# Performance work log

Measured on AMD Instinct MI355X. Metric: run time of the kernel, lower is better.

The kernel has to match this reference:

```python
import jax, jax.numpy as jnp
import numpy as np

D_MODEL = 1024
NUM_HEADS = 16
D_K = D_MODEL // NUM_HEADS
THETA = 10000.0


def _rope(x, pos):
    # x: [H, B, S, D_K]; pos: [S] int. Interleaved-pair rotation (matrix-form RoPE).
    d2 = D_K // 2
    inv_freq = THETA ** (-(2.0 * jnp.arange(d2, dtype=jnp.float32)) / D_K)  # [d2]
    ang = pos.astype(jnp.float32)[:, None] * inv_freq[None, :]              # [S, d2]
    sin, cos = jnp.sin(ang), jnp.cos(ang)
    xr = x.reshape(*x.shape[:-1], d2, 2)
    x0, x1 = xr[..., 0], xr[..., 1]
    out0 = cos * x0 - sin * x1
    out1 = sin * x0 + cos * x1
    return jnp.stack([out0, out1], axis=-1).reshape(x.shape)


def setup_inputs() -> dict:
    key = jax.random.key(0)
    ks = jax.random.split(key, 5)
    scale = 1.0 / np.sqrt(D_MODEL)
    return {
        "x": jax.random.normal(ks[0], (4, 2048, D_MODEL), dtype=jnp.float32),
        "token_positions": jnp.arange(2048, dtype=jnp.int32),
        "Wq": jax.random.normal(ks[1], (D_MODEL, D_MODEL), dtype=jnp.float32) * scale,
        "Wk": jax.random.normal(ks[2], (D_MODEL, D_MODEL), dtype=jnp.float32) * scale,
        "Wv": jax.random.normal(ks[3], (D_MODEL, D_MODEL), dtype=jnp.float32) * scale,
        "Wo": jax.random.normal(ks[4], (D_MODEL, D_MODEL), dtype=jnp.float32) * scale,
    }


def reference(x, token_positions, Wq, Wk, Wv, Wo):
    B, S, D = x.shape
    H, dk = NUM_HEADS, D_K
    # Projections (Linear stores weight [out,in], applies x @ W.T)
    def proj(W):
        return (x @ W.T).reshape(B, S, H, dk).transpose(2, 0, 1, 3)  # [H,B,S,dk]
    q, k, v = proj(Wq), proj(Wk), proj(Wv)
    q = _rope(q, token_positions)
    k = _rope(k, token_positions)
    scores = jnp.einsum("hbsd,hbtd->hbst", q, k) / jnp.sqrt(jnp.float32(dk))
    causal = jnp.tril(jnp.ones((S, S), dtype=bool))
    scores = jnp.where(causal, scores, jnp.float32(-1e9))
    attn = jax.nn.softmax(scores, axis=-1)
    out = jnp.einsum("hbst,hbtd->hbsd", attn, v)       # [H,B,S,dk]
    out = out.transpose(1, 2, 0, 3).reshape(B, S, D)   # [B,S,D]
    return out @ Wo.T
```

## Files before the change

kernel.cpp:

```cpp
#include <hip/hip_runtime.h>

typedef __bf16 bf16;
typedef bf16 bf16x8 __attribute__((ext_vector_type(8)));
typedef bf16 bf16x4 __attribute__((ext_vector_type(4)));
typedef float floatx4 __attribute__((ext_vector_type(4)));

#define D_MODEL 1024
#define SEQ     2048
#define NB      4
#define NH      16
#define DKH     64
#define ROPE_L2 0.4152410118609203f

__device__ __forceinline__ floatx4 mfma16(bf16x8 a, bf16x8 b, floatx4 c) {
  return __builtin_amdgcn_mfma_f32_16x16x32_bf16(a, b, c, 0, 0, 0);
}

__device__ __forceinline__ void gload_lds16(void* lds_uniform, const void* gsrc) {
  __builtin_amdgcn_global_load_lds(
      (__attribute__((address_space(1))) unsigned int*)(void*)(gsrc),
      (__attribute__((address_space(3))) unsigned int*)lds_uniform,
      16, 0, 0);
}

__global__ __launch_bounds__(256) void cvt_all(
    const float4* __restrict__ x,
    const float4* __restrict__ wq, const float4* __restrict__ wk,
    const float4* __restrict__ wv, const float4* __restrict__ wo,
    bf16x4* __restrict__ xb,
    bf16x4* __restrict__ b0, bf16x4* __restrict__ b1,
    bf16x4* __restrict__ b2, bf16x4* __restrict__ b3,
    const int* __restrict__ tokpos, float2* __restrict__ ropetab) {
  const int i = blockIdx.x * 256 + threadIdx.x;
  if (i < (1 << 21) + (1 << 20)) {
    const float4* src;
    bf16x4* dst;
    int off;
    if (i < (1 << 21)) {
      src = x; dst = xb; off = i;
    } else {
      const int j = i - (1 << 21);
      const int widx = j >> 18;
      off = j & ((1 << 18) - 1);
      src = (widx == 0) ? wq : (widx == 1) ? wk : (widx == 2) ? wv : wo;
      dst = (widx == 0) ? b0 : (widx == 1) ? b1 : (widx == 2) ? b2 : b3;
    }
    const float4 v = src[off];
    bf16x4 o;
    o[0] = (bf16)v.x; o[1] = (bf16)v.y; o[2] = (bf16)v.z; o[3] = (bf16)v.w;
    dst[off] = o;
  } else {
    const int k = i - (1 << 21) - (1 << 20);
    const int s = k >> 5, i2 = k & 31;
    const float ang = (float)tokpos[s] * exp2f(-(float)i2 * ROPE_L2);
    float sn, cs;
    sincosf(ang, &sn, &cs);
    ropetab[k] = make_float2(sn, cs);
  }
}

#define QK_SRC_DECL(Aptr, Bq, Bk)                                              \
  const int c_0 = w * 64 + lane;                                               \
  const int row0_ = c_0 >> 2, seg0_ = (c_0 & 3) ^ ((row0_ >> 1) & 3);          \
  const int c_1 = c_0 + 256;                                                   \
  const int row1_ = c_1 >> 2, seg1_ = (c_1 & 3) ^ ((row1_ >> 1) & 3);          \
  const bf16* asrc0 = (Aptr) + (size_t)(bm + row0_) * D_MODEL + seg0_ * 8;     \
  const bf16* asrc1 = (Aptr) + (size_t)(bm + row1_) * D_MODEL + seg1_ * 8;     \
  const bf16* bqsrc0 = (Bq) + (size_t)(bn + row0_) * D_MODEL + seg0_ * 8;      \
  const bf16* bqsrc1 = (Bq) + (size_t)(bn + row1_) * D_MODEL + seg1_ * 8;      \
  const bf16* bksrc0 = (Bk) + (size_t)(bn + row0_) * D_MODEL + seg0_ * 8;      \
  const bf16* bksrc1 = (Bk) + (size_t)(bn + row1_) * D_MODEL + seg1_ * 8;     \
  const int gsw = (g ^ ((r >> 1) & 3)) * 8;

#define QKA(buf) ((char*)LDSBUF + (buf) * 8192)
#define QKQ(buf) ((char*)LDSBUF + 16384 + (buf) * 8192)
#define QKK(buf) ((char*)LDSBUF + 32768 + (buf) * 8192)

#define QK_STAGE(buf, kk)                                                      \
  gload_lds16(QKA(buf) + (w * 64) * 16, asrc0 + (kk));                         \
  gload_lds16(QKQ(buf) + (w * 64) * 16, bqsrc0 + (kk));                        \
  gload_lds16(QKK(buf) + (w * 64) * 16, bksrc0 + (kk));                        \
  gload_lds16(QKA(buf) + (w * 64 + 256) * 16, asrc1 + (kk));                   \
  gload_lds16(QKQ(buf) + (w * 64 + 256) * 16, bqsrc1 + (kk));                  \
  gload_lds16(QKK(buf) + (w * 64 + 256) * 16, bksrc1 + (kk));

#define ROPEW(mm, nn, CV, SC)                                                  \
  _Pragma("unroll")                                                            \
  for (int reg = 0; reg < 4; ++reg) {                                          \
    const int srow = mm * 16 + g * 4 + reg;                                    \
    const int c = wc * 64 + nn * 16 + r;                                       \
    const int s_ = (bm + wr * 64 + srow) & (SEQ - 1);                          \
    const int d_ = c & 63;                                                     \
    float v = CV[reg];                                                         \
    float pp = __shfl_xor(v, 1);                                               \
    const float2 sc2 = ropetab[s_ * 32 + (d_ >> 1)];                           \
    float res = ((d_ & 1) == 0) ? (sc2.y * v - sc2.x * pp)                     \
                                : (sc2.x * pp + sc2.y * v);                    \
    res *= SC;                                                                 \
    *(bf16*)((char*)LDSBUF + srow * 272 + c * 2) = (bf16)res;                  \
  }

#define QK_EPI(A00,A01,A02,A03,A10,A11,A12,A13,A20,A21,A22,A23,A30,A31,A32,A33,\
               dst0, SC)                                                       \
  _Pragma("unroll")                                                            \
  for (int p = 0; p < 2; ++p) {                                                \
    if (wr == p) {                                                             \
      ROPEW(0, 0, A00, SC) ROPEW(0, 1, A01, SC) ROPEW(0, 2, A02, SC)           \
      ROPEW(0, 3, A03, SC) ROPEW(1, 0, A10, SC) ROPEW(1, 1, A11, SC)           \
      ROPEW(1, 2, A12, SC) ROPEW(1, 3, A13, SC) ROPEW(2, 0, A20, SC)           \
      ROPEW(2, 1, A21, SC) ROPEW(2, 2, A22, SC) ROPEW(2, 3, A23, SC)           \
      ROPEW(3, 0, A30, SC) ROPEW(3, 1, A31, SC) ROPEW(3, 2, A32, SC)           \
      ROPEW(3, 3, A33, SC)                                                     \
    }                                                                          \
    __syncthreads();                                                           \
    const int s_r = tid >> 2, quad = tid & 3;                                  \
    const int grow = bm + p * 64 + s_r;                                        \
    const int b_ = grow >> 11, s_ = grow & (SEQ - 1);                          \
    const int h_ = hbase + (quad >> 1);                                        \
    bf16* dstp = (dst0) + ((size_t)(b_ * NH + h_) * SEQ + s_) * DKH +          \
                 (quad & 1) * 32;                                              \
    _Pragma("unroll")                                                          \
    for (int j = 0; j < 4; ++j)                                                \
      *(float4*)(dstp + j * 8) =                                               \
          *(const float4*)((char*)LDSBUF + s_r * 272 + quad * 64 + j * 16);    \
    __syncthreads();                                                           \
  }

#define AS_BASE(buf) ((char*)LDSBUF + (buf) * 8192)
#define BS_BASE(buf) ((char*)LDSBUF + 16384 + (buf) * 8192)

#define GEMM_STAGE(buf, kk)                                                    \
  gload_lds16(AS_BASE(buf) + (w * 64) * 16, asrc0 + (kk));                     \
  gload_lds16(BS_BASE(buf) + (w * 64) * 16, bsrc0 + (kk));                     \
  gload_lds16(AS_BASE(buf) + (w * 64 + 256) * 16, asrc1 + (kk));               \
  gload_lds16(BS_BASE(buf) + (w * 64 + 256) * 16, bsrc1 + (kk));

#define GEMM_MAINLOOP(Aptr, Bptr)                                              \
  const int c_0 = w * 64 + lane;                                               \
  const int row0_ = c_0 >> 2, seg0_ = (c_0 & 3) ^ ((row0_ >> 1) & 3);          \
  const int c_1 = c_0 + 256;                                                   \
  const int row1_ = c_1 >> 2, seg1_ = (c_1 & 3) ^ ((row1_ >> 1) & 3);          \
  const bf16* asrc0 = (Aptr) + (size_t)(bm + row0_) * D_MODEL + seg0_ * 8;     \
  const bf16* asrc1 = (Aptr) + (size_t)(bm + row1_) * D_MODEL + seg1_ * 8;     \
  const bf16* bsrc0 = (Bptr) + (size_t)(bn + row0_) * D_MODEL + seg0_ * 8;     \
  const bf16* bsrc1 = (Bptr) + (size_t)(bn + row1_) * D_MODEL + seg1_ * 8;     \
  const int gsw = (g ^ ((r >> 1) & 3)) * 8;                                    \
  GEMM_STAGE(0, 0)                                                             \
  __syncthreads();                                                             \
  int cub = 0;                                                                 \
  for (int kt = 0; kt < 32; ++kt) {                                            \
    if (kt + 1 < 32) { GEMM_STAGE(cub ^ 1, (kt + 1) * 32) }                    \
    const bf16* Abase = (const bf16*)AS_BASE(cub) + (wr * 64 + r) * 32 + gsw;  \
    const bf16* Bbase = (const bf16*)BS_BASE(cub) + (wc * 64 + r) * 32 + gsw;  \
    bf16x8 a0 = *(const bf16x8*)(Abase + 0 * 512);                             \
    bf16x8 a1 = *(const bf16x8*)(Abase + 1 * 512);                             \
    bf16x8 a2 = *(const bf16x8*)(Abase + 2 * 512);                             \
    bf16x8 a3 = *(const bf16x8*)(Abase + 3 * 512);                             \
    bf16x8 b0 = *(const bf16x8*)(Bbase + 0 * 512);                             \
    bf16x8 b1 = *(const bf16x8*)(Bbase + 1 * 512);                             \
    bf16x8 b2 = *(const bf16x8*)(Bbase + 2 * 512);                             \
    bf16x8 b3 = *(const bf16x8*)(Bbase + 3 * 512);                             \
    __builtin_amdgcn_s_setprio(1);                                             \
    c00 = mfma16(a0, b0, c00); c01 = mfma16(a0, b1, c01);                      \
    c02 = mfma16(a0, b2, c02); c03 = mfma16(a0, b3, c03);                      \
    c10 = mfma16(a1, b0, c10); c11 = mfma16(a1, b1, c11);                      \
    c12 = mfma16(a1, b2, c12); c13 = mfma16(a1, b3, c13);                      \
    c20 = mfma16(a2, b0, c20); c21 = mfma16(a2, b1, c21);                      \
    c22 = mfma16(a2, b2, c22); c23 = mfma16(a2, b3, c23);                      \
    c30 = mfma16(a3, b0, c30); c31 = mfma16(a3, b1, c31);                      \
    c32 = mfma16(a3, b2, c32); c33 = mfma16(a3, b3, c33);                      \
    __builtin_amdgcn_s_setprio(0);                                             \
    __syncthreads();                                                           \
    cub ^= 1;                                                                  \
  }

#define V_WRITE(mm, nn, CV)                                                    \
  _Pragma("unroll")                                                            \
  for (int reg = 0; reg < 4; ++reg) {                                          \
    const int crow = nn * 16 + r;                                              \
    const int s_l = wr * 64 + mm * 16 + g * 4 + reg;                           \
    *(bf16*)((char*)LDSBUF + crow * 272 + s_l * 2) = (bf16)CV[reg];            \
  }

__global__ __launch_bounds__(256, 2) void gemm_proj(
    const bf16* __restrict__ A,
    const bf16* __restrict__ Wq, const bf16* __restrict__ Wk,
    const bf16* __restrict__ Wv,
    bf16* __restrict__ Qd, bf16* __restrict__ Kd, bf16* __restrict__ Vd,
    const float2* __restrict__ ropetab) {
  __shared__ __align__(16) char LDSBUF[49152];
  const int orig = (int)(blockIdx.x + (blockIdx.y << 3));
  const int l = (orig & 7) * 64 + (orig >> 3);
  const int bm = (l >> 3) * 128, bn = (l & 7) * 128;
  const int tid = threadIdx.x, lane = tid & 63, w = tid >> 6;
  const int wr = w >> 1, wc = w & 1;
  const int r = lane & 15, g = lane >> 4;
  const int hbase = bn >> 6;

  if (blockIdx.z == 0) {
    floatx4 q00 = {}, q01 = {}, q02 = {}, q03 = {};
    floatx4 q10 = {}, q11 = {}, q12 = {}, q13 = {};
    floatx4 q20 = {}, q21 = {}, q22 = {}, q23 = {};
    floatx4 q30 = {}, q31 = {}, q32 = {}, q33 = {};
    floatx4 k00 = {}, k01 = {}, k02 = {}, k03 = {};
    floatx4 k10 = {}, k11 = {}, k12 = {}, k13 = {};
    floatx4 k20 = {}, k21 = {}, k22 = {}, k23 = {};
    floatx4 k30 = {}, k31 = {}, k32 = {}, k33 = {};

    QK_SRC_DECL(A, Wq, Wk)
    QK_STAGE(0, 0)
    __syncthreads();
    int cub = 0;
    for (int kt = 0; kt < 32; ++kt) {
      if (kt + 1 < 32) { QK_STAGE(cub ^ 1, (kt + 1) * 32) }
      const bf16* Abase = (const bf16*)QKA(cub) + (wr * 64 + r) * 32 + gsw;
      const bf16* Qbase = (const bf16*)QKQ(cub) + (wc * 64 + r) * 32 + gsw;
      const bf16* Kbase = (const bf16*)QKK(cub) + (wc * 64 + r) * 32 + gsw;
      bf16x8 a0 = *(const bf16x8*)(Abase + 0 * 512);
      bf16x8 a1 = *(const bf16x8*)(Abase + 1 * 512);
      bf16x8 a2 = *(const bf16x8*)(Abase + 2 * 512);
      bf16x8 a3 = *(const bf16x8*)(Abase + 3 * 512);
      bf16x8 bq0 = *(const bf16x8*)(Qbase + 0 * 512);
      bf16x8 bq1 = *(const bf16x8*)(Qbase + 1 * 512);
      bf16x8 bq2 = *(const bf16x8*)(Qbase + 2 * 512);
      bf16x8 bq3 = *(const bf16x8*)(Qbase + 3 * 512);
      bf16x8 bk0 = *(const bf16x8*)(Kbase + 0 * 512);
      bf16x8 bk1 = *(const bf16x8*)(Kbase + 1 * 512);
      bf16x8 bk2 = *(const bf16x8*)(Kbase + 2 * 512);
      bf16x8 bk3 = *(const bf16x8*)(Kbase + 3 * 512);
      __builtin_amdgcn_s_setprio(1);
      q00 = mfma16(a0, bq0, q00); q01 = mfma16(a0, bq1, q01);
      q02 = mfma16(a0, bq2, q02); q03 = mfma16(a0, bq3, q03);
      k00 = mfma16(a0, bk0, k00); k01 = mfma16(a0, bk1, k01);
      k02 = mfma16(a0, bk2, k02); k03 = mfma16(a0, bk3, k03);
      q10 = mfma16(a1, bq0, q10); q11 = mfma16(a1, bq1, q11);
      q12 = mfma16(a1, bq2, q12); q13 = mfma16(a1, bq3, q13);
      k10 = mfma16(a1, bk0, k10); k11 = mfma16(a1, bk1, k11);
      k12 = mfma16(a1, bk2, k12); k13 = mfma16(a1, bk3, k13);
      q20 = mfma16(a2, bq0, q20); q21 = mfma16(a2, bq1, q21);
      q22 = mfma16(a2, bq2, q22); q23 = mfma16(a2, bq3, q23);
      k20 = mfma16(a2, bk0, k20); k21 = mfma16(a2, bk1, k21);
      k22 = mfma16(a2, bk2, k22); k23 = mfma16(a2, bk3, k23);
      q30 = mfma16(a3, bq0, q30); q31 = mfma16(a3, bq1, q31);
      q32 = mfma16(a3, bq2, q32); q33 = mfma16(a3, bq3, q33);
      k30 = mfma16(a3, bk0, k30); k31 = mfma16(a3, bk1, k31);
      k32 = mfma16(a3, bk2, k32); k33 = mfma16(a3, bk3, k33);
      __builtin_amdgcn_s_setprio(0);
      __syncthreads();
      cub ^= 1;
    }

    QK_EPI(q00,q01,q02,q03,q10,q11,q12,q13,q20,q21,q22,q23,q30,q31,q32,q33,
           Qd, 0.125f)
    QK_EPI(k00,k01,k02,k03,k10,k11,k12,k13,k20,k21,k22,k23,k30,k31,k32,k33,
           Kd, 1.0f)
  } else {
    floatx4 c00 = {}, c01 = {}, c02 = {}, c03 = {};
    floatx4 c10 = {}, c11 = {}, c12 = {}, c13 = {};
    floatx4 c20 = {}, c21 = {}, c22 = {}, c23 = {};
    floatx4 c30 = {}, c31 = {}, c32 = {}, c33 = {};
    GEMM_MAINLOOP(A, Wv)

    const int b_ = bm >> 11, sbase = bm & (SEQ - 1);
#pragma unroll
    for (int p = 0; p < 2; ++p) {
      if (wc == p) {
        V_WRITE(0, 0, c00) V_WRITE(0, 1, c01) V_WRITE(0, 2, c02) V_WRITE(0, 3, c03)
        V_WRITE(1, 0, c10) V_WRITE(1, 1, c11) V_WRITE(1, 2, c12) V_WRITE(1, 3, c13)
        V_WRITE(2, 0, c20) V_WRITE(2, 1, c21) V_WRITE(2, 2, c22) V_WRITE(2, 3, c23)
        V_WRITE(3, 0, c30) V_WRITE(3, 1, c31) V_WRITE(3, 2, c32) V_WRITE(3, 3, c33)
      }
      __syncthreads();
      const int c_r = tid >> 2, quad = tid & 3;
      const int c = p * 64 + c_r;
      const int h_ = hbase + (c >> 6), d_ = c & 63;
      bf16* dstp = Vd + ((size_t)(b_ * NH + h_) * DKH + d_) * SEQ + sbase + quad * 32;
#pragma unroll
      for (int j = 0; j < 4; ++j)
        *(float4*)(dstp + j * 8) =
            *(const float4*)((char*)LDSBUF + c_r * 272 + quad * 64 + j * 16);
      __syncthreads();
    }
  }
}

#define OUT_EPI(mm, nn, CV)                                                    \
  _Pragma("unroll")                                                            \
  for (int reg = 0; reg < 4; ++reg) {                                          \
    const int grow = bm + wr * 64 + mm * 16 + g * 4 + reg;                     \
    const int gcol = bn + wc * 64 + nn * 16 + r;                               \
    C[(size_t)grow * D_MODEL + gcol] = CV[reg];                                \
  }

__global__ __launch_bounds__(256, 3) void gemm_out(const bf16* __restrict__ A,
                                                   const bf16* __restrict__ Bw,
                                                   float* __restrict__ C) {
  __shared__ __align__(16) char LDSBUF[32768];
  const int orig = (int)(blockIdx.x + (blockIdx.y << 3));
  const int l = (orig & 7) * 64 + (orig >> 3);
  const int bm = (l >> 3) * 128, bn = (l & 7) * 128;
  const int tid = threadIdx.x, lane = tid & 63, w = tid >> 6;
  const int wr = w >> 1, wc = w & 1;
  const int r = lane & 15, g = lane >> 4;
  floatx4 c00 = {}, c01 = {}, c02 = {}, c03 = {};
  floatx4 c10 = {}, c11 = {}, c12 = {}, c13 = {};
  floatx4 c20 = {}, c21 = {}, c22 = {}, c23 = {};
  floatx4 c30 = {}, c31 = {}, c32 = {}, c33 = {};
  GEMM_MAINLOOP(A, Bw)
  OUT_EPI(0, 0, c00) OUT_EPI(0, 1, c01) OUT_EPI(0, 2, c02) OUT_EPI(0, 3, c03)
  OUT_EPI(1, 0, c10) OUT_EPI(1, 1, c11) OUT_EPI(1, 2, c12) OUT_EPI(1, 3, c13)
  OUT_EPI(2, 0, c20) OUT_EPI(2, 1, c21) OUT_EPI(2, 2, c22) OUT_EPI(2, 3, c23)
  OUT_EPI(3, 0, c30) OUT_EPI(3, 1, c31) OUT_EPI(3, 2, c32) OUT_EPI(3, 3, c33)
}

__global__ __launch_bounds__(256, 3) void attn128(const bf16* __restrict__ Q,
                                                  const bf16* __restrict__ Kk,
                                                  const bf16* __restrict__ Vt,
                                                  bf16* __restrict__ AO) {
  const int orig = (int)(blockIdx.x + (blockIdx.y << 4));
  const int i_ = orig >> 3;
  const int qt = 15 - (i_ >> 3);
  const int bh = (orig & 7) * 8 + (i_ & 7);
  const int b = bh >> 4, h = bh & 15;
  const int tid = threadIdx.x, lane = tid & 63, w = tid >> 6;
  const int r = lane & 15, g = lane >> 4;
  const int q0 = qt * 128 + w * 32;

  const bf16* Qb = Q + (size_t)bh * SEQ * DKH;
  const bf16* Kb = Kk + (size_t)bh * SEQ * DKH;
  const bf16* Vb = Vt + (size_t)bh * DKH * SEQ;

  __shared__ bf16 Ks[2][64 * 64];
  __shared__ bf16 Vs[2][64 * 64];
  __shared__ bf16 Ps[4][32 * 64];

  int ldsoff[2];
  const char* ksrc[2];
  const char* vsrc[2];
#pragma unroll
  for (int j = 0; j < 2; ++j) {
    const int L = (w * 64 + lane + 256 * j) * 16;
    const int S = L ^ (((L >> 7) & 7) << 4);
    ldsoff[j] = (w * 64 + 256 * j) * 16;
    ksrc[j] = (const char*)Kb + S;
    vsrc[j] = (const char*)Vb + (size_t)(S >> 7) * (SEQ * 2) + (S & 127);
  }

#define ATTN_STAGE(buf, tt)                                                   \
  _Pragma("unroll")                                                           \
  for (int j = 0; j < 2; ++j) {                                               \
    gload_lds16((char*)Ks[buf] + ldsoff[j], ksrc[j] + (size_t)(tt) * 8192);   \
    gload_lds16((char*)Vs[buf] + ldsoff[j], vsrc[j] + (size_t)(tt) * 128);    \
  }

#define SM_TILE(MASKED)                                                        \
  _Pragma("unroll")                                                            \
  for (int m = 0; m < 2; ++m) {                                                \
    const int qq_ = q0 + m * 16 + r;                                           \
    const int wl_ = m * 16 + r;                                                \
    _Pragma("unroll")                                                          \
    for (int nf = 0; nf < 4; ++nf) {                                           \
      floatx4 p;                                                               \
      _Pragma("unroll")                                                        \
      for (int reg = 0; reg < 4; ++reg) {                                      \
        float pe = exp2f(fmaf(sc[m][nf][reg], 1.442695041f, -17.31234049f));   \
        if (MASKED && (t0 + nf * 16 + g * 4 + reg > qq_)) pe = 0.f;            \
        p[reg] = pe;                                                           \
      }                                                                        \
      l2[m] += p;                                                              \
      unsigned u0, u1;                                                         \
      asm("v_cvt_pk_bf16_f32 %0, %1, %2" : "=v"(u0) : "v"(p[0]), "v"(p[1]));   \
      asm("v_cvt_pk_bf16_f32 %0, %1, %2" : "=v"(u1) : "v"(p[2]), "v"(p[3]));   \
      const int pb = (wl_ * 128 + nf * 32 + g * 8) ^ ((wl_ & 7) << 4);         \
      *(uint2*)((char*)Ps[w] + pb) = make_uint2(u0, u1);                       \
    }                                                                          \
  }

  bf16x8 qf[2][2];
#pragma unroll
  for (int m = 0; m < 2; ++m)
#pragma unroll
    for (int ks = 0; ks < 2; ++ks)
      qf[m][ks] = *(const bf16x8*)(Qb + (size_t)(q0 + m * 16 + r) * DKH + ks * 32 + g * 8);

  floatx4 o[2][4] = {};
  floatx4 l2[2] = {};

  const int nt = 2 * qt + 2;
  ATTN_STAGE(0, 0)
  __syncthreads();
  int cu = 0;
  for (int t = 0; t < nt; ++t) {
    if (t + 1 < nt) ATTN_STAGE(cu ^ 1, t + 1)
    const int t0 = t * 64;

    floatx4 sc[2][4];
    __builtin_amdgcn_s_setprio(1);
#pragma unroll
    for (int nf = 0; nf < 4; ++nf) {
      const int row = nf * 16 + r;
      const int off0 = (row * 128 + g * 16) ^ ((row & 7) << 4);
      bf16x8 kf0 = *(const bf16x8*)((const char*)Ks[cu] + off0);
      bf16x8 kf1 = *(const bf16x8*)((const char*)Ks[cu] + (off0 ^ 64));
      sc[0][nf] = mfma16(kf1, qf[0][1], mfma16(kf0, qf[0][0], floatx4{0.f, 0.f, 0.f, 0.f}));
      sc[1][nf] = mfma16(kf1, qf[1][1], mfma16(kf0, qf[1][0], floatx4{0.f, 0.f, 0.f, 0.f}));
    }
    __builtin_amdgcn_s_setprio(0);

    const bool edge = (t0 + 63 > q0);
    if (edge) {
      SM_TILE(1)
    } else {
      SM_TILE(0)
    }
    asm volatile("s_waitcnt lgkmcnt(0)" ::: "memory");

    bf16x8 pf[2][2];
#pragma unroll
    for (int m = 0; m < 2; ++m)
#pragma unroll
      for (int ks = 0; ks < 2; ++ks) {
        const int prow = m * 16 + r;
        const int ab = (prow * 128 + ks * 64 + g * 16) ^ ((prow & 7) << 4);
        pf[m][ks] = *(const bf16x8*)((const char*)Ps[w] + ab);
      }
    __builtin_amdgcn_s_setprio(1);
#pragma unroll
    for (int nf = 0; nf < 4; ++nf) {
      const int vrow = nf * 16 + r;
      const int vb0 = (vrow * 128 + g * 16) ^ ((vrow & 7) << 4);
      bf16x8 vf0 = *(const bf16x8*)((const char*)Vs[cu] + vb0);
      bf16x8 vf1 = *(const bf16x8*)((const char*)Vs[cu] + (vb0 ^ 64));
#pragma unroll
      for (int m = 0; m < 2; ++m)
        o[m][nf] = mfma16(pf[m][1], vf1, mfma16(pf[m][0], vf0, o[m][nf]));
    }
    __builtin_amdgcn_s_setprio(0);
    __syncthreads();
    cu ^= 1;
  }

  float lsm[2];
#pragma unroll
  for (int m = 0; m < 2; ++m) {
    float ls = l2[m][0] + l2[m][1] + l2[m][2] + l2[m][3];
    ls += __shfl_xor(ls, 16);
    ls += __shfl_xor(ls, 32);
    lsm[m] = ls;
  }
  float linv[2][4];
#pragma unroll
  for (int m = 0; m < 2; ++m)
#pragma unroll
    for (int reg = 0; reg < 4; ++reg)
      linv[m][reg] = 1.f / __shfl(lsm[m], g * 4 + reg);

#pragma unroll
  for (int m = 0; m < 2; ++m)
#pragma unroll
    for (int nf = 0; nf < 4; ++nf)
#pragma unroll
      for (int reg = 0; reg < 4; ++reg) {
        const int s = q0 + m * 16 + g * 4 + reg;
        const int d = nf * 16 + r;
        const float val = o[m][nf][reg] * linv[m][reg];
        AO[((size_t)(b * SEQ + s)) * D_MODEL + h * DKH + d] = (bf16)val;
      }
}

extern "C" void kernel_launch(void* const* d_in, const int* in_sizes, int n_in,
                              void* d_out, int out_size, void* d_ws, size_t ws_size,
                              hipStream_t stream) {
  const float* x = (const float*)d_in[0];
  const int* tokpos = (const int*)d_in[1];
  const float* Wq = (const float*)d_in[2];
  const float* Wk = (const float*)d_in[3];
  const float* Wv = (const float*)d_in[4];
  const float* Wo = (const float*)d_in[5];
  float* out = (float*)d_out;

  char* ws = (char*)d_ws;
  if (ws_size < (72ull << 20)) return;

  bf16* xb  = (bf16*)(ws);
  bf16* wb0 = (bf16*)(ws + (16ull << 20));
  bf16* wb1 = (bf16*)(ws + (18ull << 20));
  bf16* wb2 = (bf16*)(ws + (20ull << 20));
  bf16* wb3 = (bf16*)(ws + (22ull << 20));
  bf16* Qb  = (bf16*)(ws + (24ull << 20));
  bf16* Kb  = (bf16*)(ws + (40ull << 20));
  bf16* Vt  = (bf16*)(ws + (56ull << 20));
  bf16* AO  = (bf16*)(ws);
  float2* ropetab = (float2*)d_out;

  cvt_all<<<12544, 256, 0, stream>>>((const float4*)x, (const float4*)Wq,
                                     (const float4*)Wk, (const float4*)Wv,
                                     (const float4*)Wo, (bf16x4*)xb,
                                     (bf16x4*)wb0, (bf16x4*)wb1,
                                     (bf16x4*)wb2, (bf16x4*)wb3,
                                     tokpos, ropetab);

  gemm_proj<<<dim3(8, 64, 2), 256, 0, stream>>>(xb, wb0, wb1, wb2,
                                                Qb, Kb, Vt, ropetab);
  attn128<<<dim3(16, 64), 256, 0, stream>>>(Qb, Kb, Vt, AO);
  gemm_out<<<dim3(8, 64), 256, 0, stream>>>(AO, wb3, out);
}
```

Baseline: 171.3 us.

## Split fused QK projection into per-head 64-wide tiles to balance work with V blocks

The Q/K projection blocks now cover a 128x64 tile (one head) for both Wq and Wk instead of 128x128, so each QK block does the same MFMA work as a V block. The grid changes to a flat 1536-block launch in which two of every three blocks are QK blocks, with swizzled block indexing. LDS use drops from 48KB to 32KB, which can raise occupancy. The cost is that each A tile is loaded from memory twice as often for QK, and there are more blocks and epilogue barriers.

New measurement: 187.8 us. 9.6% more time.

```diff
diff --git a/kernel.cpp b/kernel.cpp
--- a/kernel.cpp
+++ b/kernel.cpp
@@ -59,70 +59,51 @@
   }
 }
 
-#define QK_SRC_DECL(Aptr, Bq, Bk)                                              \
-  const int c_0 = w * 64 + lane;                                               \
-  const int row0_ = c_0 >> 2, seg0_ = (c_0 & 3) ^ ((row0_ >> 1) & 3);          \
-  const int c_1 = c_0 + 256;                                                   \
-  const int row1_ = c_1 >> 2, seg1_ = (c_1 & 3) ^ ((row1_ >> 1) & 3);          \
-  const bf16* asrc0 = (Aptr) + (size_t)(bm + row0_) * D_MODEL + seg0_ * 8;     \
-  const bf16* asrc1 = (Aptr) + (size_t)(bm + row1_) * D_MODEL + seg1_ * 8;     \
-  const bf16* bqsrc0 = (Bq) + (size_t)(bn + row0_) * D_MODEL + seg0_ * 8;      \
-  const bf16* bqsrc1 = (Bq) + (size_t)(bn + row1_) * D_MODEL + seg1_ * 8;      \
-  const bf16* bksrc0 = (Bk) + (size_t)(bn + row0_) * D_MODEL + seg0_ * 8;      \
-  const bf16* bksrc1 = (Bk) + (size_t)(bn + row1_) * D_MODEL + seg1_ * 8;     \
-  const int gsw = (g ^ ((r >> 1) & 3)) * 8;
-
-#define QKA(buf) ((char*)LDSBUF + (buf) * 8192)
-#define QKQ(buf) ((char*)LDSBUF + 16384 + (buf) * 8192)
-#define QKK(buf) ((char*)LDSBUF + 32768 + (buf) * 8192)
-
-#define QK_STAGE(buf, kk)                                                      \
-  gload_lds16(QKA(buf) + (w * 64) * 16, asrc0 + (kk));                         \
-  gload_lds16(QKQ(buf) + (w * 64) * 16, bqsrc0 + (kk));                        \
-  gload_lds16(QKK(buf) + (w * 64) * 16, bksrc0 + (kk));                        \
-  gload_lds16(QKA(buf) + (w * 64 + 256) * 16, asrc1 + (kk));                   \
-  gload_lds16(QKQ(buf) + (w * 64 + 256) * 16, bqsrc1 + (kk));                  \
-  gload_lds16(QKK(buf) + (w * 64 + 256) * 16, bksrc1 + (kk));
-
-#define ROPEW(mm, nn, CV, SC)                                                  \
+
+#define QK64A(buf) ((char*)LDSBUF + (buf) * 16384)
+#define QK64Q(buf) ((char*)LDSBUF + (buf) * 16384 + 8192)
+#define QK64K(buf) ((char*)LDSBUF + (buf) * 16384 + 12288)
+
+#define QK64_STAGE(buf, kk)                                                    \
+  gload_lds16(QK64A(buf) + (w * 64) * 16, asrc0 + (kk));                       \
+  gload_lds16(QK64A(buf) + (w * 64 + 256) * 16, asrc1 + (kk));                 \
+  gload_lds16(QK64Q(buf) + (w * 64) * 16, bqsrc + (kk));                       \
+  gload_lds16(QK64K(buf) + (w * 64) * 16, bksrc + (kk));
+
+#define ROPEW64(mm, nn, CV, SC)                                                \
   _Pragma("unroll")                                                            \
   for (int reg = 0; reg < 4; ++reg) {                                          \
     const int srow = mm * 16 + g * 4 + reg;                                    \
-    const int c = wc * 64 + nn * 16 + r;                                       \
-    const int s_ = (bm + wr * 64 + srow) & (SEQ - 1);                          \
-    const int d_ = c & 63;                                                     \
+    const int col = wc * 32 + nn * 16 + r;                                     \
+    const int s_ = (bm + p * 64 + srow) & (SEQ - 1);                           \
     float v = CV[reg];                                                         \
     float pp = __shfl_xor(v, 1);                                               \
-    const float2 sc2 = ropetab[s_ * 32 + (d_ >> 1)];                           \
-    float res = ((d_ & 1) == 0) ? (sc2.y * v - sc2.x * pp)                     \
-                                : (sc2.x * pp + sc2.y * v);                    \
+    const float2 sc2 = ropetab[s_ * 32 + (col >> 1)];                          \
+    float res = ((col & 1) == 0) ? (sc2.y * v - sc2.x * pp)                    \
+                                 : (sc2.x * pp + sc2.y * v);                   \
     res *= SC;                                                                 \
-    *(bf16*)((char*)LDSBUF + srow * 272 + c * 2) = (bf16)res;                  \
-  }
-
-#define QK_EPI(A00,A01,A02,A03,A10,A11,A12,A13,A20,A21,A22,A23,A30,A31,A32,A33,\
-               dst0, SC)                                                       \
+    *(bf16*)((char*)LDSBUF + srow * 272 + col * 2) = (bf16)res;                \
+  }
+
+#define QK64_EPI(A00,A01,A10,A11,A20,A21,A30,A31, dst0, SC)                    \
   _Pragma("unroll")                                                            \
   for (int p = 0; p < 2; ++p) {                                                \
     if (wr == p) {                                                             \
-      ROPEW(0, 0, A00, SC) ROPEW(0, 1, A01, SC) ROPEW(0, 2, A02, SC)           \
-      ROPEW(0, 3, A03, SC) ROPEW(1, 0, A10, SC) ROPEW(1, 1, A11, SC)           \
-      ROPEW(1, 2, A12, SC) ROPEW(1, 3, A13, SC) ROPEW(2, 0, A20, SC)           \
-      ROPEW(2, 1, A21, SC) ROPEW(2, 2, A22, SC) ROPEW(2, 3, A23, SC)           \
-      ROPEW(3, 0, A30, SC) ROPEW(3, 1, A31, SC) ROPEW(3, 2, A32, SC)           \
-      ROPEW(3, 3, A33, SC)                                                     \
+      ROPEW64(0, 0, A00, SC) ROPEW64(0, 1, A01, SC)                            \
+      ROPEW64(1, 0, A10, SC) ROPEW64(1, 1, A11, SC)                            \
+      ROPEW64(2, 0, A20, SC) ROPEW64(2, 1, A21, SC)                            \
+      ROPEW64(3, 0, A30, SC) ROPEW64(3, 1, A31, SC)                            \
     }                                                                          \
     __syncthreads();                                                           \
     const int s_r = tid >> 2, quad = tid & 3;                                  \
     const int grow = bm + p * 64 + s_r;                                        \
     const int b_ = grow >> 11, s_ = grow & (SEQ - 1);                          \
-    const int h_ = hbase + (quad >> 1);                                        \
-    bf16* dstp = (dst0) + ((size_t)(b_ * NH + h_) * SEQ + s_) * DKH +          \
-                 (quad & 1) * 32;                                              \
+    bf16* dstp = (dst0) + ((size_t)(b_ * NH + h) * SEQ + s_) * DKH +           \
+                 quad * 16;                                                    \
     _Pragma("unroll")                                                          \
-    for (int j = 0; j < 4; ++j)                                                \
+    for (int j = 0; j < 2; ++j)                                                \
       *(float4*)(dstp + j * 8) =                                               \
-          *(const float4*)((char*)LDSBUF + s_r * 272 + quad * 64 + j * 16);    \
+          *(const float4*)((char*)LDSBUF + s_r * 272 + quad * 32 + j * 16);    \
     __syncthreads();                                                           \
   }
 
@@ -188,73 +169,71 @@
     const bf16* __restrict__ Wv,
     bf16* __restrict__ Qd, bf16* __restrict__ Kd, bf16* __restrict__ Vd,
     const float2* __restrict__ ropetab) {
-  __shared__ __align__(16) char LDSBUF[49152];
-  const int orig = (int)(blockIdx.x + (blockIdx.y << 3));
-  const int l = (orig & 7) * 64 + (orig >> 3);
-  const int bm = (l >> 3) * 128, bn = (l & 7) * 128;
+  __shared__ __align__(16) char LDSBUF[32768];
+  const int orig = (int)(blockIdx.x + (blockIdx.y << 4));
+  const int l = (orig & 7) * 192 + (orig >> 3);
+  const int grp = l / 3, rem = l - grp * 3;
   const int tid = threadIdx.x, lane = tid & 63, w = tid >> 6;
   const int wr = w >> 1, wc = w & 1;
   const int r = lane & 15, g = lane >> 4;
-  const int hbase = bn >> 6;
-
-  if (blockIdx.z == 0) {
-    floatx4 q00 = {}, q01 = {}, q02 = {}, q03 = {};
-    floatx4 q10 = {}, q11 = {}, q12 = {}, q13 = {};
-    floatx4 q20 = {}, q21 = {}, q22 = {}, q23 = {};
-    floatx4 q30 = {}, q31 = {}, q32 = {}, q33 = {};
-    floatx4 k00 = {}, k01 = {}, k02 = {}, k03 = {};
-    floatx4 k10 = {}, k11 = {}, k12 = {}, k13 = {};
-    floatx4 k20 = {}, k21 = {}, k22 = {}, k23 = {};
-    floatx4 k30 = {}, k31 = {}, k32 = {}, k33 = {};
-
-    QK_SRC_DECL(A, Wq, Wk)
-    QK_STAGE(0, 0)
+
+  if (rem < 2) {
+    const int id = grp * 2 + rem;
+    const int bm = (id >> 4) * 128;
+    const int h = id & 15;
+    const int bn = h * 64;
+
+    const int ar0 = tid >> 2, as0 = (tid & 3) ^ ((ar0 >> 1) & 3);
+    const int cA1 = tid + 256;
+    const int ar1 = cA1 >> 2, as1 = (cA1 & 3) ^ ((ar1 >> 1) & 3);
+    const bf16* asrc0 = A + (size_t)(bm + ar0) * D_MODEL + as0 * 8;
+    const bf16* asrc1 = A + (size_t)(bm + ar1) * D_MODEL + as1 * 8;
+    const int br = tid >> 2, bs = (tid & 3) ^ ((br >> 1) & 3);
+    const bf16* bqsrc = Wq + (size_t)(bn + br) * D_MODEL + bs * 8;
+    const bf16* bksrc = Wk + (size_t)(bn + br) * D_MODEL + bs * 8;
+    const int gsw = (g ^ ((r >> 1) & 3)) * 8;
+
+    floatx4 q00 = {}, q01 = {}, q10 = {}, q11 = {};
+    floatx4 q20 = {}, q21 = {}, q30 = {}, q31 = {};
+    floatx4 k00 = {}, k01 = {}, k10 = {}, k11 = {};
+    floatx4 k20 = {}, k21 = {}, k30 = {}, k31 = {};
+
+    QK64_STAGE(0, 0)
     __syncthreads();
     int cub = 0;
     for (int kt = 0; kt < 32; ++kt) {
-      if (kt + 1 < 32) { QK_STAGE(cub ^ 1, (kt + 1) * 32) }
-      const bf16* Abase = (const bf16*)QKA(cub) + (wr * 64 + r) * 32 + gsw;
-      const bf16* Qbase = (const bf16*)QKQ(cub) + (wc * 64 + r) * 32 + gsw;
-      const bf16* Kbase = (const bf16*)QKK(cub) + (wc * 64 + r) * 32 + gsw;
+      if (kt + 1 < 32) { QK64_STAGE(cub ^ 1, (kt + 1) * 32) }
+      const bf16* Abase = (const bf16*)QK64A(cub) + (wr * 64 + r) * 32 + gsw;
+      const bf16* Qbase = (const bf16*)QK64Q(cub) + (wc * 32 + r) * 32 + gsw;
+      const bf16* Kbase = (const bf16*)QK64K(cub) + (wc * 32 + r) * 32 + gsw;
       bf16x8 a0 = *(const bf16x8*)(Abase + 0 * 512);
       bf16x8 a1 = *(const bf16x8*)(Abase + 1 * 512);
       bf16x8 a2 = *(const bf16x8*)(Abase + 2 * 512);
       bf16x8 a3 = *(const bf16x8*)(Abase + 3 * 512);
       bf16x8 bq0 = *(const bf16x8*)(Qbase + 0 * 512);
       bf16x8 bq1 = *(const bf16x8*)(Qbase + 1 * 512);
-      bf16x8 bq2 = *(const bf16x8*)(Qbase + 2 * 512);
-      bf16x8 bq3 = *(const bf16x8*)(Qbase + 3 * 512);
       bf16x8 bk0 = *(const bf16x8*)(Kbase + 0 * 512);
       bf16x8 bk1 = *(const bf16x8*)(Kbase + 1 * 512);
-      bf16x8 bk2 = *(const bf16x8*)(Kbase + 2 * 512);
-      bf16x8 bk3 = *(const bf16x8*)(Kbase + 3 * 512);
       __builtin_amdgcn_s_setprio(1);
       q00 = mfma16(a0, bq0, q00); q01 = mfma16(a0, bq1, q01);
-      q02 = mfma16(a0, bq2, q02); q03 = mfma16(a0, bq3, q03);
       k00 = mfma16(a0, bk0, k00); k01 = mfma16(a0, bk1, k01);
-      k02 = mfma16(a0, bk2, k02); k03 = mfma16(a0, bk3, k03);
       q10 = mfma16(a1, bq0, q10); q11 = mfma16(a1, bq1, q11);
-      q12 = mfma16(a1, bq2, q12); q13 = mfma16(a1, bq3, q13);
       k10 = mfma16(a1, bk0, k10); k11 = mfma16(a1, bk1, k11);
-      k12 = mfma16(a1, bk2, k12); k13 = mfma16(a1, bk3, k13);
       q20 = mfma16(a2, bq0, q20); q21 = mfma16(a2, bq1, q21);
-      q22 = mfma16(a2, bq2, q22); q23 = mfma16(a2, bq3, q23);
       k20 = mfma16(a2, bk0, k20); k21 = mfma16(a2, bk1, k21);
-      k22 = mfma16(a2, bk2, k22); k23 = mfma16(a2, bk3, k23);
       q30 = mfma16(a3, bq0, q30); q31 = mfma16(a3, bq1, q31);
-      q32 = mfma16(a3, bq2, q32); q33 = mfma16(a3, bq3, q33);
       k30 = mfma16(a3, bk0, k30); k31 = mfma16(a3, bk1, k31);
-      k32 = mfma16(a3, bk2, k32); k33 = mfma16(a3, bk3, k33);
       __builtin_amdgcn_s_setprio(0);
       __syncthreads();
       cub ^= 1;
     }
 
-    QK_EPI(q00,q01,q02,q03,q10,q11,q12,q13,q20,q21,q22,q23,q30,q31,q32,q33,
-           Qd, 0.125f)
-    QK_EPI(k00,k01,k02,k03,k10,k11,k12,k13,k20,k21,k22,k23,k30,k31,k32,k33,
-           Kd, 1.0f)
+    QK64_EPI(q00, q01, q10, q11, q20, q21, q30, q31, Qd, 0.125f)
+    QK64_EPI(k00, k01, k10, k11, k20, k21, k30, k31, Kd, 1.0f)
   } else {
+    const int id = grp;
+    const int bm = (id >> 3) * 128, bn = (id & 7) * 128;
+    const int hbase = bn >> 6;
     floatx4 c00 = {}, c01 = {}, c02 = {}, c03 = {};
     floatx4 c10 = {}, c11 = {}, c12 = {}, c13 = {};
     floatx4 c20 = {}, c21 = {}, c22 = {}, c23 = {};
@@ -500,8 +479,8 @@
                                      (bf16x4*)wb2, (bf16x4*)wb3,
                                      tokpos, ropetab);
 
-  gemm_proj<<<dim3(8, 64, 2), 256, 0, stream>>>(xb, wb0, wb1, wb2,
-                                                Qb, Kb, Vt, ropetab);
+  gemm_proj<<<dim3(16, 96), 256, 0, stream>>>(xb, wb0, wb1, wb2,
+                                              Qb, Kb, Vt, ropetab);
   attn128<<<dim3(16, 64), 256, 0, stream>>>(Qb, Kb, Vt, AO);
   gemm_out<<<dim3(8, 64), 256, 0, stream>>>(AO, wb3, out);
 }
```
